# Kernel tuning notes

Hardware: AMD Instinct MI355X
Metric: run time of the kernel (lower is better)

Reference implementation:

```python
import jax, jax.numpy as jnp
import numpy as np

B, N, C, H, W = 64, 500, 256, 64, 64


def grid_sample_bilinear(im, pts):
    """torch.grid_sample bilinear, align_corners=True, padding_mode='zeros'.
    im: [B,C,H,W]; pts: [B,N,2] (x,y) in [-1,1] -> [B,C,N]."""
    b, c, h, w = im.shape
    x = (pts[..., 0] + 1.0) * 0.5 * (w - 1)  # [B,N]
    y = (pts[..., 1] + 1.0) * 0.5 * (h - 1)
    x0 = jnp.floor(x); y0 = jnp.floor(y)
    x1 = x0 + 1.0; y1 = y0 + 1.0
    wx1 = x - x0; wx0 = 1.0 - wx1
    wy1 = y - y0; wy0 = 1.0 - wy1
    flat = im.reshape(b, c, h * w)

    def gather(xi, yi):
        inb = (xi >= 0) & (xi <= w - 1) & (yi >= 0) & (yi <= h - 1)
        xc = jnp.clip(xi, 0, w - 1).astype(jnp.int32)
        yc = jnp.clip(yi, 0, h - 1).astype(jnp.int32)
        idx = (yc * w + xc)[:, None, :]  # [B,1,N]
        g = jnp.take_along_axis(flat, idx, axis=2)  # [B,C,N]
        return g * inb[:, None, :].astype(im.dtype)

    return (gather(x0, y0) * (wx0 * wy0)[:, None, :]
            + gather(x1, y0) * (wx1 * wy0)[:, None, :]
            + gather(x0, y1) * (wx0 * wy1)[:, None, :]
            + gather(x1, y1) * (wx1 * wy1)[:, None, :])


def setup_inputs() -> dict:
    key = jax.random.key(0)
    ks = jax.random.split(key, 12)
    p = jax.random.uniform(ks[0], (B, N, 2), jnp.float32, -1.0, 1.0)
    s_feat = jax.random.normal(ks[1], (B, C, H, W), jnp.float32)
    def conv_p(k, co, ci):
        k1, k2 = jax.random.split(k)
        s = 1.0 / np.sqrt(ci)
        return (jax.random.uniform(k1, (co, ci), jnp.float32, -s, s),
                jax.random.uniform(k2, (co,), jnp.float32, -s, s))
    w0, b0 = conv_p(ks[2], 128, 256)
    w1, b1 = conv_p(ks[3], 64, 128 + 256)
    w2, b2 = conv_p(ks[4], 5, 64 + 256)
    fc_w, fc_b = conv_p(ks[5], 236, 5 * N)
    return {"p": p, "s_feat": s_feat, "w0": w0, "b0": b0, "w1": w1, "b1": b1,
            "w2": w2, "b2": b2, "fc_w": fc_w, "fc_b": fc_b}


def reference(p, s_feat, w0, b0, w1, b1, w2, b2, fc_w, fc_b):
    feat = grid_sample_bilinear(s_feat, p)  # [B,256,N]
    y = jnp.einsum('oc,bcn->bon', w0, feat) + b0[None, :, None]
    y = jax.nn.leaky_relu(y, 0.01)
    y = jnp.einsum('oc,bcn->bon', w1, jnp.concatenate([y, feat], axis=1)) + b1[None, :, None]
    y = jax.nn.leaky_relu(y, 0.01)
    y = jnp.einsum('oc,bcn->bon', w2, jnp.concatenate([y, feat], axis=1)) + b2[None, :, None]
    y = jax.nn.relu(y)           # last_op
    y = y.reshape(y.shape[0], -1)  # [B, 5*N]
    return y @ fc_w.T + fc_b       # [B, 236]
```

## Files before the change

### kernel.cpp

```cpp
#include <hip/hip_runtime.h>
#include <hip/hip_bf16.h>

#define BB 64
#define NN 500
#define CC 256
#define HH 64
#define WW 64
#define HWSZ 4096
#define NPTS 32000
#define NPAD 512

typedef __attribute__((ext_vector_type(4))) short s4v;
typedef __attribute__((ext_vector_type(8))) short s8v;
typedef __attribute__((ext_vector_type(4))) float f4v;
typedef __attribute__((ext_vector_type(4))) int i4v;

__device__ __forceinline__ unsigned short bfround(float f) {
    unsigned u = __builtin_bit_cast(unsigned, f);
    return (unsigned short)((u + 0x7FFFu + ((u >> 16) & 1u)) >> 16);
}

#define GATHER_BLKS 2048
#define NCHB 8
#define NBUF 3
#define W0F_N 32768
#define W1F_N 24576
#define W2F_N 5120
#define PACK_N (W0F_N + W1F_N + W2F_N)
#define PACK_BLKS ((PACK_N + 511) / 512)
#define TR_BLKS (40 * 4)
#define TOTAL_BLKS (GATHER_BLKS + PACK_BLKS + TR_BLKS)

__global__ __launch_bounds__(512) void k_gp(const float* __restrict__ sfeat,
                                            const float* __restrict__ pts,
                                            const float* __restrict__ w0,
                                            const float* __restrict__ w1,
                                            const float* __restrict__ w2,
                                            const float* __restrict__ fcw,
                                            unsigned int* __restrict__ featB,
                                            unsigned short* __restrict__ w0f,
                                            unsigned short* __restrict__ w1f,
                                            unsigned short* __restrict__ w2f,
                                            float* __restrict__ fcwT) {
    __shared__ float im[NBUF][HWSZ];
    const int blk = blockIdx.x;
    const int tid = threadIdx.x;

    if (blk >= GATHER_BLKS + PACK_BLKS) {
        float (*tile)[65] = (float(*)[65])im;
        const int tb = blk - (GATHER_BLKS + PACK_BLKS);
        const int kt = tb % 40, ot = tb / 40;
        const int k0 = kt * 64, o0 = ot * 64;
        for (int i = tid; i < 64 * 64; i += 512) {
            int oo = i >> 6, kk = i & 63;
            int o = o0 + oo, k = k0 + kk;
            tile[oo][kk] = (o < 236 && k < 2500) ? fcw[(size_t)o * 2500 + k] : 0.f;
        }
        __syncthreads();
        for (int i = tid; i < 64 * 64; i += 512) {
            int kk = i >> 6, oo = i & 63;
            int o = o0 + oo, k = k0 + kk;
            if (o < 236 && k < 2500) fcwT[(size_t)k * 236 + o] = tile[oo][kk];
        }
        return;
    }

    if (blk >= GATHER_BLKS) {
        int i = (blk - GATHER_BLKS) * 512 + tid;
        if (i < W0F_N) {
            int j = i & 7, ll = (i >> 3) & 63, s = (i >> 9) & 7, m = i >> 12;
            int row = m * 16 + (ll & 15), k = s * 32 + (ll >> 4) * 8 + j;
            w0f[i] = bfround(w0[row * 256 + k]);
        } else if (i < W0F_N + W1F_N) {
            int d = i - W0F_N;
            int j = d & 7, ll = (d >> 3) & 63, rest = d >> 9;
            int s = rest % 12, m = rest / 12;
            int row = m * 16 + (ll & 15), k = s * 32 + (ll >> 4) * 8 + j;
            w1f[d] = bfround(w1[row * 384 + k]);
        } else if (i < PACK_N) {
            int d = i - (W0F_N + W1F_N);
            int j = d & 7, ll = (d >> 3) & 63, s = d >> 9;
            int row = ll & 15, k = s * 32 + (ll >> 4) * 8 + j;
            float v = (row < 5) ? w2[row * 320 + k] : 0.f;
            w2f[d] = bfround(v);
        }
        return;
    }

    const int b     = blk >> 5;
    const int chunk = blk & 31;
    const int ch0   = chunk * NCHB;
    const int n     = tid;

    int4 id = make_int4(0, 0, 0, 0);
    float4 wt = make_float4(0.f, 0.f, 0.f, 0.f);
    if (n < NN) {
        float x = (pts[((size_t)b * NN + n) * 2 + 0] + 1.f) * 0.5f * (float)(WW - 1);
        float y = (pts[((size_t)b * NN + n) * 2 + 1] + 1.f) * 0.5f * (float)(HH - 1);
        float x0f = floorf(x), y0f = floorf(y);
        float x1f = x0f + 1.f, y1f = y0f + 1.f;
        float wx1 = x - x0f, wx0 = 1.f - wx1;
        float wy1 = y - y0f, wy0 = 1.f - wy1;
        float mx0 = (x0f >= 0.f && x0f <= (float)(WW - 1)) ? 1.f : 0.f;
        float mx1 = (x1f >= 0.f && x1f <= (float)(WW - 1)) ? 1.f : 0.f;
        float my0 = (y0f >= 0.f && y0f <= (float)(HH - 1)) ? 1.f : 0.f;
        float my1 = (y1f >= 0.f && y1f <= (float)(HH - 1)) ? 1.f : 0.f;
        int x0 = (int)fminf(fmaxf(x0f, 0.f), (float)(WW - 1));
        int x1 = (int)fminf(fmaxf(x1f, 0.f), (float)(WW - 1));
        int y0 = (int)fminf(fmaxf(y0f, 0.f), (float)(HH - 1));
        int y1 = (int)fminf(fmaxf(y1f, 0.f), (float)(HH - 1));
        id = make_int4(y0 * WW + x0, y0 * WW + x1, y1 * WW + x0, y1 * WW + x1);
        wt = make_float4(wx0 * wy0 * mx0 * my0, wx1 * wy0 * mx1 * my0,
                         wx0 * wy1 * mx0 * my1, wx1 * wy1 * mx1 * my1);
    }

    const float4* src = (const float4*)(sfeat + ((size_t)b * CC + ch0) * HWSZ);

#define ISSUE_CH(T, BUF)                                                      \
    {                                                                         \
        const float4* s2 = src + (size_t)(T) * (HWSZ / 4);                    \
        float4* dst = (float4*)im[BUF];                                       \
        _Pragma("unroll")                                                     \
        for (int it = 0; it < 2; it++) {                                      \
            int j = it * 512 + tid;                                           \
            __builtin_amdgcn_global_load_lds(                                 \
                (const __attribute__((address_space(1))) void*)(s2 + j),      \
                (__attribute__((address_space(3))) void*)(dst + j),           \
                16, 0, 0);                                                    \
        }                                                                     \
    }

    ISSUE_CH(0, 0);
    ISSUE_CH(1, 1);

    unsigned short hprev = 0;
    for (int t = 0; t < NCHB; t++) {
        if (t + 2 < NCHB) {
            ISSUE_CH(t + 2, (t + 2) % 3);
            asm volatile("s_waitcnt vmcnt(4)" ::: "memory");
        } else if (t + 1 < NCHB) {
            asm volatile("s_waitcnt vmcnt(2)" ::: "memory");
        } else {
            asm volatile("s_waitcnt vmcnt(0)" ::: "memory");
        }
        asm volatile("s_barrier" ::: "memory");

        if (n < NN) {
            const float* L = im[t % 3];
            float r = wt.x * L[id.x] + wt.y * L[id.y] + wt.z * L[id.z] + wt.w * L[id.w];
            unsigned short h = bfround(r);
            if (t & 1) {
                unsigned int v = (unsigned int)hprev | ((unsigned int)h << 16);
                featB[(((size_t)b * 32 + chunk) * 4 + (t >> 1)) * 512 + n] = v;
            } else {
                hprev = h;
            }
        }
        if (t + 1 < NCHB)
            asm volatile("s_barrier" ::: "memory");
    }
#undef ISSUE_CH
}

#define K1_S 136
#define K2_S 72

__device__ __forceinline__ s8v mkfrag(const unsigned short* p) {
    return *(const s8v*)p;
}

__global__ __launch_bounds__(512, 4) void k_mlp(const unsigned int* __restrict__ featB,
                                                const unsigned short* __restrict__ w0f,
                                                const unsigned short* __restrict__ w1f,
                                                const unsigned short* __restrict__ w2f,
                                                const float* __restrict__ b0,
                                                const float* __restrict__ b1,
                                                const float* __restrict__ b2,
                                                float* __restrict__ y2f) {
    __shared__ unsigned short c1B[64 * K1_S];
    __shared__ unsigned short c2B[64 * K2_S];

    const int b   = blockIdx.y;
    const int n0  = blockIdx.x * 64;
    const int tid = threadIdx.x;
    const int w   = tid >> 6, l = tid & 63;
    const int nt  = w & 3, mh = w >> 2;
    const int lo16 = l & 15, hi = l >> 4;
    const int c = nt * 16 + lo16;

    s8v bhs[8];
    const unsigned int* fb = featB + (size_t)b * (32 * 4 * 512) + (n0 + c);
#pragma unroll
    for (int s = 0; s < 8; s++) {
        const int kg = s * 4 + hi;
        i4v hx;
#pragma unroll
        for (int t = 0; t < 4; t++)
            hx[t] = (int)fb[(size_t)(kg * 4 + t) * 512];
        bhs[s] = __builtin_bit_cast(s8v, hx);
    }

    f4v acc[4];
#pragma unroll
    for (int q = 0; q < 4; q++) acc[q] = (f4v){0.f, 0.f, 0.f, 0.f};
#pragma unroll
    for (int s = 0; s < 8; s++) {
#pragma unroll
        for (int q = 0; q < 4; q++) {
            const s8v a = mkfrag(w0f + ((size_t)((mh * 4 + q) * 8 + s) * 64 + l) * 8);
            acc[q] = __builtin_amdgcn_mfma_f32_16x16x32_bf16(a, bhs[s], acc[q], 0, 0, 0);
        }
    }
#pragma unroll
    for (int q = 0; q < 4; q++) {
#pragma unroll
        for (int r = 0; r < 4; r++) {
            int ch = (mh * 4 + q) * 16 + hi * 4 + r;
            float v = acc[q][r] + b0[ch];
            v = v > 0.f ? v : 0.01f * v;
            c1B[c * K1_S + ch] = bfround(v);
        }
    }
    __syncthreads();

    f4v accA[2];
#pragma unroll
    for (int q = 0; q < 2; q++) accA[q] = (f4v){0.f, 0.f, 0.f, 0.f};
#pragma unroll
    for (int s = 0; s < 4; s++) {
        const s8v bh = *(const s8v*)&c1B[c * K1_S + s * 32 + hi * 8];
#pragma unroll
        for (int q = 0; q < 2; q++) {
            const s8v a = mkfrag(w1f + ((size_t)((mh * 2 + q) * 12 + s) * 64 + l) * 8);
            accA[q] = __builtin_amdgcn_mfma_f32_16x16x32_bf16(a, bh, accA[q], 0, 0, 0);
        }
    }
#pragma unroll
    for (int s = 4; s < 12; s++) {
#pragma unroll
        for (int q = 0; q < 2; q++) {
            const s8v a = mkfrag(w1f + ((size_t)((mh * 2 + q) * 12 + s) * 64 + l) * 8);
            accA[q] = __builtin_amdgcn_mfma_f32_16x16x32_bf16(a, bhs[s - 4], accA[q], 0, 0, 0);
        }
    }
#pragma unroll
    for (int q = 0; q < 2; q++) {
#pragma unroll
        for (int r = 0; r < 4; r++) {
            int ch = (mh * 2 + q) * 16 + hi * 4 + r;
            float v = accA[q][r] + b1[ch];
            v = v > 0.f ? v : 0.01f * v;
            c2B[c * K2_S + ch] = bfround(v);
        }
    }
    __syncthreads();

    if (mh == 0) {
        f4v acc2 = {0.f, 0.f, 0.f, 0.f};
#pragma unroll
        for (int s = 0; s < 2; s++) {
            const s8v bh = *(const s8v*)&c2B[c * K2_S + s * 32 + hi * 8];
            const s8v a  = mkfrag(w2f + ((size_t)s * 64 + l) * 8);
            acc2 = __builtin_amdgcn_mfma_f32_16x16x32_bf16(a, bh, acc2, 0, 0, 0);
        }
#pragma unroll
        for (int s = 2; s < 10; s++) {
            const s8v a = mkfrag(w2f + ((size_t)s * 64 + l) * 8);
            acc2 = __builtin_amdgcn_mfma_f32_16x16x32_bf16(a, bhs[s - 2], acc2, 0, 0, 0);
        }
#pragma unroll
        for (int r = 0; r < 4; r++) {
            int ch = hi * 4 + r;
            if (ch < 5) {
                float v = acc2[r] + b2[ch];
                v = fmaxf(v, 0.f);
                int n = n0 + c;
                if (n < NN) y2f[(size_t)b * 2500 + ch * NN + n] = v;
            }
        }
    }
}

__global__ __launch_bounds__(256) void k_fc1(const float* __restrict__ y2f,
                                             const float* __restrict__ fcwT,
                                             float* __restrict__ part) {
    __shared__ float ys[313];
    const int b  = blockIdx.x & 63;
    const int kc = blockIdx.x >> 6;
    const int start = kc * 312 + (kc < 4 ? kc : 4);
    const int len   = (kc < 4) ? 313 : 312;
    const float* yb = y2f + (size_t)b * 2500 + start;
    for (int j = threadIdx.x; j < len; j += 256) ys[j] = yb[j];
    __syncthreads();
    const int o = threadIdx.x;
    if (o < 236) {
        float acc = 0.f;
        const float* wp = fcwT + (size_t)start * 236 + o;
#pragma unroll 8
        for (int k = 0; k < len; k++) acc = fmaf(wp[(size_t)k * 236], ys[k], acc);
        part[((size_t)kc * 64 + b) * 236 + o] = acc;
    }
}

__global__ __launch_bounds__(256) void k_fc2(const float* __restrict__ part,
                                             const float* __restrict__ fcb,
                                             float* __restrict__ out) {
    const int b = blockIdx.x;
    const int o = threadIdx.x;
    if (o < 236) {
        float acc = fcb[o];
#pragma unroll
        for (int kc = 0; kc < 8; kc++) acc += part[((size_t)kc * 64 + b) * 236 + o];
        out[b * 236 + o] = acc;
    }
}

extern "C" void kernel_launch(void* const* d_in, const int* in_sizes, int n_in,
                              void* d_out, int out_size, void* d_ws, size_t ws_size,
                              hipStream_t stream) {
    const float* p   = (const float*)d_in[0];
    const float* sf  = (const float*)d_in[1];
    const float* w0  = (const float*)d_in[2];
    const float* b0  = (const float*)d_in[3];
    const float* w1  = (const float*)d_in[4];
    const float* b1  = (const float*)d_in[5];
    const float* w2  = (const float*)d_in[6];
    const float* b2  = (const float*)d_in[7];
    const float* fcw = (const float*)d_in[8];
    const float* fcb = (const float*)d_in[9];
    float* out = (float*)d_out;

    char* ws = (char*)d_ws;
    unsigned int*   featB = (unsigned int*)(ws);
    float*          y2f   = (float*)(ws + 16777216);
    float*          fcwT  = (float*)(ws + 17417216);
    float*          part  = (float*)(ws + 19777216);
    unsigned short* w0f   = (unsigned short*)(ws + 20260544);
    unsigned short* w1f   = (unsigned short*)(ws + 20326080);
    unsigned short* w2f   = (unsigned short*)(ws + 20375232);

    k_gp<<<TOTAL_BLKS, 512, 0, stream>>>(sf, p, w0, w1, w2, fcw,
                                         featB, w0f, w1f, w2f, fcwT);
    k_mlp<<<dim3(8, BB), 512, 0, stream>>>(featB, w0f, w1f, w2f,
                                           b0, b1, b2, y2f);
    k_fc1<<<512, 256, 0, stream>>>(y2f, fcwT, part);
    k_fc2<<<BB, 256, 0, stream>>>(part, fcb, out);
}
```

Measured before the change: 79.62 us.

## Halve gather block size with two points per thread and double-buffered LDS

The gather/pack kernel drops from 512 to 256 threads per block, and each thread now handles two sample points. The LDS staging ring shrinks from three channel buffers to two, so prefetch depth falls from two channels ahead to one. The smaller per-block LDS footprint is meant to let more blocks share a CU and hide global-to-LDS latency across blocks rather than within one. The cost is a shallower per-block pipeline and more per-thread work and registers.

```diff
diff --git a/kernel.cpp b/kernel.cpp
--- a/kernel.cpp
+++ b/kernel.cpp
@@ -20,18 +20,38 @@
     return (unsigned short)((u + 0x7FFFu + ((u >> 16) & 1u)) >> 16);
 }
 
+__device__ __forceinline__ void prep_point(const float* __restrict__ pts,
+                                           int b, int n, int4& id, float4& wt) {
+    float x = (pts[((size_t)b * NN + n) * 2 + 0] + 1.f) * 0.5f * (float)(WW - 1);
+    float y = (pts[((size_t)b * NN + n) * 2 + 1] + 1.f) * 0.5f * (float)(HH - 1);
+    float x0f = floorf(x), y0f = floorf(y);
+    float x1f = x0f + 1.f, y1f = y0f + 1.f;
+    float wx1 = x - x0f, wx0 = 1.f - wx1;
+    float wy1 = y - y0f, wy0 = 1.f - wy1;
+    float mx0 = (x0f >= 0.f && x0f <= (float)(WW - 1)) ? 1.f : 0.f;
+    float mx1 = (x1f >= 0.f && x1f <= (float)(WW - 1)) ? 1.f : 0.f;
+    float my0 = (y0f >= 0.f && y0f <= (float)(HH - 1)) ? 1.f : 0.f;
+    float my1 = (y1f >= 0.f && y1f <= (float)(HH - 1)) ? 1.f : 0.f;
+    int x0 = (int)fminf(fmaxf(x0f, 0.f), (float)(WW - 1));
+    int x1 = (int)fminf(fmaxf(x1f, 0.f), (float)(WW - 1));
+    int y0 = (int)fminf(fmaxf(y0f, 0.f), (float)(HH - 1));
+    int y1 = (int)fminf(fmaxf(y1f, 0.f), (float)(HH - 1));
+    id = make_int4(y0 * WW + x0, y0 * WW + x1, y1 * WW + x0, y1 * WW + x1);
+    wt = make_float4(wx0 * wy0 * mx0 * my0, wx1 * wy0 * mx1 * my0,
+                     wx0 * wy1 * mx0 * my1, wx1 * wy1 * mx1 * my1);
+}
+
 #define GATHER_BLKS 2048
 #define NCHB 8
-#define NBUF 3
 #define W0F_N 32768
 #define W1F_N 24576
 #define W2F_N 5120
 #define PACK_N (W0F_N + W1F_N + W2F_N)
-#define PACK_BLKS ((PACK_N + 511) / 512)
+#define PACK_BLKS ((PACK_N + 255) / 256)
 #define TR_BLKS (40 * 4)
 #define TOTAL_BLKS (GATHER_BLKS + PACK_BLKS + TR_BLKS)
 
-__global__ __launch_bounds__(512) void k_gp(const float* __restrict__ sfeat,
+__global__ __launch_bounds__(256) void k_gp(const float* __restrict__ sfeat,
                                             const float* __restrict__ pts,
                                             const float* __restrict__ w0,
                                             const float* __restrict__ w1,
@@ -42,7 +62,7 @@
                                             unsigned short* __restrict__ w1f,
                                             unsigned short* __restrict__ w2f,
                                             float* __restrict__ fcwT) {
-    __shared__ float im[NBUF][HWSZ];
+    __shared__ float im[2][HWSZ];
     const int blk = blockIdx.x;
     const int tid = threadIdx.x;
 
@@ -51,13 +71,13 @@
         const int tb = blk - (GATHER_BLKS + PACK_BLKS);
         const int kt = tb % 40, ot = tb / 40;
         const int k0 = kt * 64, o0 = ot * 64;
-        for (int i = tid; i < 64 * 64; i += 512) {
+        for (int i = tid; i < 64 * 64; i += 256) {
             int oo = i >> 6, kk = i & 63;
             int o = o0 + oo, k = k0 + kk;
             tile[oo][kk] = (o < 236 && k < 2500) ? fcw[(size_t)o * 2500 + k] : 0.f;
         }
         __syncthreads();
-        for (int i = tid; i < 64 * 64; i += 512) {
+        for (int i = tid; i < 64 * 64; i += 256) {
             int kk = i >> 6, oo = i & 63;
             int o = o0 + oo, k = k0 + kk;
             if (o < 236 && k < 2500) fcwT[(size_t)k * 236 + o] = tile[oo][kk];
@@ -66,7 +86,7 @@
     }
 
     if (blk >= GATHER_BLKS) {
-        int i = (blk - GATHER_BLKS) * 512 + tid;
+        int i = (blk - GATHER_BLKS) * 256 + tid;
         if (i < W0F_N) {
             int j = i & 7, ll = (i >> 3) & 63, s = (i >> 9) & 7, m = i >> 12;
             int row = m * 16 + (ll & 15), k = s * 32 + (ll >> 4) * 8 + j;
@@ -90,29 +110,13 @@
     const int b     = blk >> 5;
     const int chunk = blk & 31;
     const int ch0   = chunk * NCHB;
-    const int n     = tid;
-
-    int4 id = make_int4(0, 0, 0, 0);
-    float4 wt = make_float4(0.f, 0.f, 0.f, 0.f);
-    if (n < NN) {
-        float x = (pts[((size_t)b * NN + n) * 2 + 0] + 1.f) * 0.5f * (float)(WW - 1);
-        float y = (pts[((size_t)b * NN + n) * 2 + 1] + 1.f) * 0.5f * (float)(HH - 1);
-        float x0f = floorf(x), y0f = floorf(y);
-        float x1f = x0f + 1.f, y1f = y0f + 1.f;
-        float wx1 = x - x0f, wx0 = 1.f - wx1;
-        float wy1 = y - y0f, wy0 = 1.f - wy1;
-        float mx0 = (x0f >= 0.f && x0f <= (float)(WW - 1)) ? 1.f : 0.f;
-        float mx1 = (x1f >= 0.f && x1f <= (float)(WW - 1)) ? 1.f : 0.f;
-        float my0 = (y0f >= 0.f && y0f <= (float)(HH - 1)) ? 1.f : 0.f;
-        float my1 = (y1f >= 0.f && y1f <= (float)(HH - 1)) ? 1.f : 0.f;
-        int x0 = (int)fminf(fmaxf(x0f, 0.f), (float)(WW - 1));
-        int x1 = (int)fminf(fmaxf(x1f, 0.f), (float)(WW - 1));
-        int y0 = (int)fminf(fmaxf(y0f, 0.f), (float)(HH - 1));
-        int y1 = (int)fminf(fmaxf(y1f, 0.f), (float)(HH - 1));
-        id = make_int4(y0 * WW + x0, y0 * WW + x1, y1 * WW + x0, y1 * WW + x1);
-        wt = make_float4(wx0 * wy0 * mx0 * my0, wx1 * wy0 * mx1 * my0,
-                         wx0 * wy1 * mx0 * my1, wx1 * wy1 * mx1 * my1);
-    }
+    const int n0p   = tid;
+    const int n1p   = tid + 256;
+
+    int4 id0, id1 = make_int4(0, 0, 0, 0);
+    float4 wt0, wt1 = make_float4(0.f, 0.f, 0.f, 0.f);
+    prep_point(pts, b, n0p, id0, wt0);
+    if (n1p < NN) prep_point(pts, b, n1p, id1, wt1);
 
     const float4* src = (const float4*)(sfeat + ((size_t)b * CC + ch0) * HWSZ);
 
@@ -121,8 +125,8 @@
         const float4* s2 = src + (size_t)(T) * (HWSZ / 4);                    \
         float4* dst = (float4*)im[BUF];                                       \
         _Pragma("unroll")                                                     \
-        for (int it = 0; it < 2; it++) {                                      \
-            int j = it * 512 + tid;                                           \
+        for (int it = 0; it < 4; it++) {                                      \
+            int j = it * 256 + tid;                                           \
             __builtin_amdgcn_global_load_lds(                                 \
                 (const __attribute__((address_space(1))) void*)(s2 + j),      \
                 (__attribute__((address_space(3))) void*)(dst + j),           \
@@ -131,30 +135,34 @@
     }
 
     ISSUE_CH(0, 0);
-    ISSUE_CH(1, 1);
-
-    unsigned short hprev = 0;
+
+    unsigned short hprev0 = 0, hprev1 = 0;
     for (int t = 0; t < NCHB; t++) {
-        if (t + 2 < NCHB) {
-            ISSUE_CH(t + 2, (t + 2) % 3);
+        if (t + 1 < NCHB) {
+            ISSUE_CH(t + 1, (t + 1) & 1);
             asm volatile("s_waitcnt vmcnt(4)" ::: "memory");
-        } else if (t + 1 < NCHB) {
-            asm volatile("s_waitcnt vmcnt(2)" ::: "memory");
         } else {
             asm volatile("s_waitcnt vmcnt(0)" ::: "memory");
         }
         asm volatile("s_barrier" ::: "memory");
 
-        if (n < NN) {
-            const float* L = im[t % 3];
-            float r = wt.x * L[id.x] + wt.y * L[id.y] + wt.z * L[id.z] + wt.w * L[id.w];
-            unsigned short h = bfround(r);
-            if (t & 1) {
-                unsigned int v = (unsigned int)hprev | ((unsigned int)h << 16);
-                featB[(((size_t)b * 32 + chunk) * 4 + (t >> 1)) * 512 + n] = v;
-            } else {
-                hprev = h;
-            }
+        const float* L = im[t & 1];
+        float r0 = wt0.x * L[id0.x] + wt0.y * L[id0.y] +
+                   wt0.z * L[id0.z] + wt0.w * L[id0.w];
+        unsigned short h0 = bfround(r0);
+        unsigned short h1 = 0;
+        if (n1p < NN) {
+            float r1 = wt1.x * L[id1.x] + wt1.y * L[id1.y] +
+                       wt1.z * L[id1.z] + wt1.w * L[id1.w];
+            h1 = bfround(r1);
+        }
+        if (t & 1) {
+            size_t base = (((size_t)b * 32 + chunk) * 4 + (t >> 1)) * 512;
+            featB[base + n0p] = (unsigned int)hprev0 | ((unsigned int)h0 << 16);
+            if (n1p < NN)
+                featB[base + n1p] = (unsigned int)hprev1 | ((unsigned int)h1 << 16);
+        } else {
+            hprev0 = h0; hprev1 = h1;
         }
         if (t + 1 < NCHB)
             asm volatile("s_barrier" ::: "memory");
@@ -339,7 +347,7 @@
     unsigned short* w1f   = (unsigned short*)(ws + 20326080);
     unsigned short* w2f   = (unsigned short*)(ws + 20375232);
 
-    k_gp<<<TOTAL_BLKS, 512, 0, stream>>>(sf, p, w0, w1, w2, fcw,
+    k_gp<<<TOTAL_BLKS, 256, 0, stream>>>(sf, p, w0, w1, w2, fcw,
                                          featB, w0f, w1f, w2f, fcwT);
     k_mlp<<<dim3(8, BB), 512, 0, stream>>>(featB, w0f, w1f, w2f,
                                            b0, b1, b2, y2f);
```

Result: slower. 85.04 us (+6.8%).
